# Kernel tuning notes

Hardware: AMD Instinct MI355X
Metric: run time of the kernel (lower is better)

## Reference

```python
import jax, jax.numpy as jnp
import numpy as np

X_LIST = [256, 256, 1024, 1024, 512]
LABEL_DIM = 8
MAX_SEQ_LEN = 64
B = 256
EMB = 128
ATTR = 64
HID = 512
LAYERS = 4


def setup_inputs() -> dict:
    key = jax.random.key(0)
    ki = iter(jax.random.split(key, 80))
    def nrm(shape):
        return jax.random.normal(next(ki), shape, jnp.float32) * 0.02
    inp = {}
    inp['label'] = jax.random.normal(next(ki), (B, LABEL_DIM), jnp.float32)
    inp['length'] = jax.random.randint(next(ki), (B,), 1, MAX_SEQ_LEN + 1)
    inp['x'] = jnp.stack([jax.random.randint(next(ki), (B, MAX_SEQ_LEN), 0, v) for v in X_LIST], axis=-1)
    inp['x_now'] = jnp.stack([jax.random.randint(next(ki), (B, MAX_SEQ_LEN), 0, v) for v in X_LIST], axis=-1)
    for i, v in enumerate(X_LIST):
        inp[f'emb{i}'] = nrm((v, EMB))
    inp['pad_emb'] = jnp.zeros((1, ATTR), jnp.float32)
    for i in range(len(X_LIST) - 1):
        inp[f'cond_W{i}'] = nrm((ATTR, (i + 1) * EMB))
        inp[f'cond_b{i}'] = jnp.zeros((ATTR,), jnp.float32)
    inp['len_W'] = nrm((64, MAX_SEQ_LEN))
    inp['len_b'] = jnp.zeros((64,), jnp.float32)
    comb_in = EMB * len(X_LIST) + 64  # 704
    inp['comb_W'] = nrm((LABEL_DIM, HID, comb_in))
    inp['comb_b'] = jnp.zeros((LABEL_DIM, HID), jnp.float32)
    inp['lstm_Wih'] = nrm((LAYERS, 4 * HID, HID))
    inp['lstm_Whh'] = nrm((LAYERS, 4 * HID, HID))
    inp['lstm_bih'] = jnp.zeros((LAYERS, 4 * HID), jnp.float32)
    inp['lstm_bhh'] = jnp.zeros((LAYERS, 4 * HID), jnp.float32)
    for i, v in enumerate(X_LIST):
        inp[f'out_W{i}'] = nrm((v, HID + ATTR))
        inp[f'out_b{i}'] = jnp.zeros((v,), jnp.float32)
    return inp


def _forward(label, emb0, emb1, emb2, emb3, emb4, pad_emb,
             cond_W0, cond_W1, cond_W2, cond_W3, cond_b0, cond_b1, cond_b2, cond_b3,
             len_W, len_b, comb_W, comb_b,
             lstm_Wih, lstm_Whh, lstm_bih, lstm_bhh,
             out_W0, out_W1, out_W2, out_W3, out_W4,
             out_b0, out_b1, out_b2, out_b3, out_b4,
             length, x, x_now):
    embs = [emb0, emb1, emb2, emb3, emb4]
    cond_W = [cond_W0, cond_W1, cond_W2, cond_W3]
    cond_b = [cond_b0, cond_b1, cond_b2, cond_b3]
    out_W = [out_W0, out_W1, out_W2, out_W3, out_W4]
    out_b = [out_b0, out_b1, out_b2, out_b3, out_b4]
    Bn, T, _ = x.shape
    # length branch: one_hot(length-1) -> Linear -> ReLU -> [B, 64]
    length_oh = jax.nn.one_hot(length - 1, MAX_SEQ_LEN, dtype=jnp.float32)
    length_out = jax.nn.relu(length_oh @ len_W.T + len_b)
    # per-attribute embedding lookups, concat -> [B, T, 5*128]
    emb_list = jnp.concatenate([embs[i][x[:, :, i]] for i in range(len(X_LIST))], axis=2)
    now_emb = jnp.concatenate([embs[i][x_now[:, :, i]] for i in range(len(X_LIST) - 1)], axis=2)
    # condition features: pad for head 0, small MLPs on prefixes of now_emb
    attr = [jnp.broadcast_to(pad_emb, (Bn, T, ATTR))]
    for i in range(len(X_LIST) - 1):
        attr.append(jax.nn.relu(now_emb[:, :, :(i + 1) * EMB] @ cond_W[i].T + cond_b[i]))
    combined = jnp.concatenate(
        [emb_list, jnp.broadcast_to(length_out[:, None, :], (Bn, T, 64))], axis=2)  # [B,T,704]
    # label-routed combine_fc: compute all LABEL_DIM branches, gather matching branch
    fc = jax.nn.relu(jnp.einsum('btd,lhd->blth', combined, comb_W) + comb_b[None, :, None, :])
    label_int = jnp.argmax(label, axis=1)
    combined_out = jnp.take_along_axis(fc, label_int[:, None, None, None], axis=1)[:, 0]  # [B,T,H]
    # 4-layer LSTM, torch gate order (i,f,g,o), zero initial state
    xs = combined_out.transpose(1, 0, 2)  # [T,B,H]
    for l in range(LAYERS):
        Wih_T = lstm_Wih[l].T
        Whh_T = lstm_Whh[l].T
        bias = lstm_bih[l] + lstm_bhh[l]
        def step(carry, xt, Wih_T=Wih_T, Whh_T=Whh_T, bias=bias):
            h, c = carry
            g = xt @ Wih_T + h @ Whh_T + bias
            gi, gf, gg, go = jnp.split(g, 4, axis=-1)
            c = jax.nn.sigmoid(gf) * c + jax.nn.sigmoid(gi) * jnp.tanh(gg)
            h = jax.nn.sigmoid(go) * jnp.tanh(c)
            return (h, c), h
        z = jnp.zeros((Bn, HID), xs.dtype)
        _, xs = jax.lax.scan(step, (z, z), xs)
    hidden = xs.transpose(1, 0, 2)  # [B,T,H]
    # per-attribute log-softmax heads over [hidden ; attr_i]
    preds = [jax.nn.log_softmax(
        jnp.concatenate([hidden, attr[i]], axis=-1) @ out_W[i].T + out_b[i], axis=-1)
        for i in range(len(X_LIST))]
    return jnp.concatenate(preds, axis=-1)  # [B, T, sum(X_LIST)]


def reference(label, emb0, emb1, emb2, emb3, emb4, pad_emb,
              cond_W0, cond_W1, cond_W2, cond_W3, cond_b0, cond_b1, cond_b2, cond_b3,
              len_W, len_b, comb_W, comb_b,
              lstm_Wih, lstm_Whh, lstm_bih, lstm_bhh,
              out_W0, out_W1, out_W2, out_W3, out_W4,
              out_b0, out_b1, out_b2, out_b3, out_b4,
              length, x, x_now):
    return _forward(label, emb0, emb1, emb2, emb3, emb4, pad_emb,
                    cond_W0, cond_W1, cond_W2, cond_W3, cond_b0, cond_b1, cond_b2, cond_b3,
                    len_W, len_b, comb_W, comb_b,
                    lstm_Wih, lstm_Whh, lstm_bih, lstm_bhh,
                    out_W0, out_W1, out_W2, out_W3, out_W4,
                    out_b0, out_b1, out_b2, out_b3, out_b4,
                    length, x, x_now)
```

## Files before the change

kernel.cpp:

```cpp
#include <hip/hip_runtime.h>
#include <math.h>


#define B_    256
#define T_    64
#define EMB_  128
#define HID_  512
#define G4_   2048
#define CIN_  704
#define HA_   576
#define ROW_  3072
#define OFF_HA 2048
#define OFF_HB 2560

#define WSUB_  256
#define WKC_   2048
#define HB0_   16384
#define SMEM_F 20480

#define BAR_T(tau) (64 + (tau) * 32)

struct Params {
  const float* label; const int* length; const int* x; const int* xnow;
  const float* emb[5]; const float* pad;
  const float* condW[4]; const float* condB[4];
  const float* lenW; const float* lenB;
  const float* combW; const float* combB;
  const float* Wih; const float* Whh; const float* bih; const float* bhh;
  const float* outW[5]; const float* outB[5];
  unsigned int* bar;
  float* out;
};

__device__ __forceinline__ void multi_barrier(unsigned int* cnt, unsigned int* gen,
                                              unsigned int n) {
  __syncthreads();
  if (threadIdx.x == 0) {
    unsigned int g = __hip_atomic_load(gen, __ATOMIC_RELAXED, __HIP_MEMORY_SCOPE_AGENT);
    unsigned int a = __hip_atomic_fetch_add(cnt, 1u, __ATOMIC_ACQ_REL, __HIP_MEMORY_SCOPE_AGENT);
    if (a == n - 1u) {
      __hip_atomic_store(cnt, 0u, __ATOMIC_RELAXED, __HIP_MEMORY_SCOPE_AGENT);
      __hip_atomic_store(gen, g + 1u, __ATOMIC_RELEASE, __HIP_MEMORY_SCOPE_AGENT);
    } else {
      while (__hip_atomic_load(gen, __ATOMIC_RELAXED, __HIP_MEMORY_SCOPE_AGENT) == g) {
        __builtin_amdgcn_s_sleep(2);
      }
      (void)__hip_atomic_load(gen, __ATOMIC_ACQUIRE, __HIP_MEMORY_SCOPE_AGENT);
    }
  }
  __syncthreads();
}

#define WRSLAB(SL) do { \
  _Pragma("unroll") \
  for (int qq = 0; qq < 8; ++qq) { \
    int cc = ((qq + lo) & 7) * 4; \
    *(float4*)&(SL)[lo * 32 + cc] = \
      make_float4(acc[qq][0], acc[qq][1], acc[qq][2], acc[qq][3]); \
  } } while (0)

#define RDSLAB(SL) do { \
  _Pragma("unroll") \
  for (int qq = 0; qq < 8; ++qq) { \
    int cc = ((qq + lo) & 7) * 4; \
    float4 vv = *(const float4*)&(SL)[lo * 32 + cc]; \
    acc[qq][0] += vv.x; acc[qq][1] += vv.y; \
    acc[qq][2] += vv.z; acc[qq][3] += vv.w; \
  } } while (0)

__global__ __launch_bounds__(256) void k_t1(Params P, int l) {
  __shared__ float sm[4608];
  const int out_off = (l & 1) ? OFF_HA : OFF_HB;
  const float* Wih = P.Wih + (size_t)l * G4_ * HID_;
  const int tid = threadIdx.x, blk = blockIdx.x;
  const int rt = blk >> 4, kt = blk & 15;
  const int r0 = rt * 128, k0 = kt * 32;
  const int ul = tid >> 3, kl = (tid & 7) * 4;
  #pragma unroll
  for (int p = 0; p < 4; ++p) {
    float4 v = *(const float4*)(Wih + (size_t)(r0 + p * 32 + ul) * HID_ + k0 + kl);
    *(float4*)&sm[(p * 32 + ul) * 36 + kl] = v;
  }
  __syncthreads();
  const int kk = tid >> 3, qb = (tid & 7) * 4;
  #pragma unroll
  for (int p = 0; p < 4; ++p) {
    int rl = qb + p * 32;
    float4 v = make_float4(sm[(rl + 0) * 36 + kk], sm[(rl + 1) * 36 + kk],
                           sm[(rl + 2) * 36 + kk], sm[(rl + 3) * 36 + kk]);
    int kabs = k0 + kk;
    int row = (r0 >> 8) * 256 + (kabs >> 1);
    int col = out_off + (kabs & 1) * 256 + (r0 & 255) + rl;
    *(float4*)&P.out[(size_t)row * ROW_ + col] = v;
  }
}

__global__ __launch_bounds__(256, 3) void k_gih(Params P, int l) {
  const int in_off  = (l & 1) ? OFF_HB : OFF_HA;
  const int out_off = (l & 1) ? OFF_HA : OFF_HB;
  const int tid = threadIdx.x;
  const int rg = tid & 63, mh = tid >> 6;
  const int rb = blockIdx.x >> 1, ch = blockIdx.x & 1;
  const int m_base = rb * 32;
  const float* arow[8];
  #pragma unroll
  for (int mm = 0; mm < 8; ++mm)
    arow[mm] = P.out + (size_t)(m_base + mh * 8 + mm) * ROW_ + in_off;
  for (int p0 = 0; p0 < 4; ++p0) {
    const int p = ch * 4 + p0;
    float acc[4][8];
    #pragma unroll
    for (int c = 0; c < 4; ++c)
      #pragma unroll
      for (int m = 0; m < 8; ++m) acc[c][m] = 0.f;
    const float* wp = P.out + (size_t)(p * 256) * ROW_ + out_off + rg * 4;
    for (int kq = 0; kq < 64; ++kq) {
      float4 w0 = *(const float4*)(wp);
      float4 w1 = *(const float4*)(wp + 256);
      float4 w2 = *(const float4*)(wp + ROW_);
      float4 w3 = *(const float4*)(wp + ROW_ + 256);
      #pragma unroll
      for (int mm = 0; mm < 8; ++mm) {
        float4 a = *(const float4*)(arow[mm] + kq * 4);
        acc[0][mm] += w0.x * a.x + w1.x * a.y + w2.x * a.z + w3.x * a.w;
        acc[1][mm] += w0.y * a.x + w1.y * a.y + w2.y * a.z + w3.y * a.w;
        acc[2][mm] += w0.z * a.x + w1.z * a.y + w2.z * a.z + w3.z * a.w;
        acc[3][mm] += w0.w * a.x + w1.w * a.y + w2.w * a.z + w3.w * a.w;
      }
      wp += 2 * ROW_;
    }
    int r4 = p * 256 + rg * 4;
    float4 bi = *(const float4*)(P.bih + l * G4_ + r4);
    float4 bh = *(const float4*)(P.bhh + l * G4_ + r4);
    float bx = bi.x + bh.x, by = bi.y + bh.y, bz = bi.z + bh.z, bw = bi.w + bh.w;
    #pragma unroll
    for (int mm = 0; mm < 8; ++mm) {
      int m = m_base + mh * 8 + mm;
      *(float4*)&P.out[(size_t)m * ROW_ + r4] =
        make_float4(acc[0][mm] + bx, acc[1][mm] + by,
                    acc[2][mm] + bz, acc[3][mm] + bw);
    }
  }
}

__global__ __launch_bounds__(256, 2) void k_lstmB(Params P, int l) {
  __shared__ float smem[SMEM_F];
  unsigned int* bar = P.bar;
  const int tid = threadIdx.x;
  const int blk = blockIdx.x;
  const int team = blk & 7, member = blk >> 3;
  const int out_off = (l & 1) ? OFF_HA : OFF_HB;

  const int kb  = tid >> 5;
  const int sgq = (tid >> 3) & 3;
  const int rg  = tid & 7;
  const bool owner = (tid < 32);
  const int s_base = team * 32 + sgq * 8;
  const int ucol0  = member * 8 + rg;

  {
    const float* Wl = P.Whh + (size_t)l * G4_ * HID_;
    const int r = tid >> 3, q = tid & 7;
    const float* src = Wl + (size_t)((r & 3) * 512 + member * 8 + (r >> 2)) * HID_
                       + q * 64;
    for (int j = 0; j < 16; ++j) {
      float4 v = *(const float4*)(src + j * 4);
      int k0 = q * 64 + j * 4;
      #pragma unroll
      for (int e = 0; e < 4; ++e) {
        int k = k0 + e;
        smem[(k >> 6) * WKC_ + ((k >> 3) & 7) * WSUB_ + (k & 7) * 32 + r] = (&v.x)[e];
      }
    }
  }
  __syncthreads();

  float cst[8];

  if (owner) {
    #pragma unroll
    for (int sj = 0; sj < 8; ++sj) {
      const size_t grow = (size_t)((s_base + sj) * 64 + 0) * ROW_;
      float zi = P.out[grow + 0 * 512 + ucol0];
      float zg = P.out[grow + 2 * 512 + ucol0];
      float zo = P.out[grow + 3 * 512 + ucol0];
      float si = 1.f / (1.f + expf(-zi));
      float so = 1.f / (1.f + expf(-zo));
      float cn = si * tanhf(zg);
      cst[sj] = cn;
      P.out[grow + out_off + ucol0] = so * tanhf(cn);
    }
  }

  for (int t = 1; t < T_; ++t) {
    multi_barrier(&bar[BAR_T(team)], &bar[BAR_T(team) + 16], 64);

    float Gp[8][4];
    if (owner) {
      #pragma unroll
      for (int sj = 0; sj < 8; ++sj) {
        const size_t grow = (size_t)((s_base + sj) * 64 + t) * ROW_;
        #pragma unroll
        for (int g = 0; g < 4; ++g)
          Gp[sj][g] = P.out[grow + g * 512 + ucol0];
      }
    }

    float acc[8][4];
    #pragma unroll
    for (int a = 0; a < 8; ++a)
      #pragma unroll
      for (int b = 0; b < 4; ++b) acc[a][b] = 0.f;

    const int idx0 = tid * 2, idx1 = idx0 + 1;
    const int s0 = idx0 >> 4, kq0 = idx0 & 15;
    const int s1 = idx1 >> 4, kq1 = idx1 & 15;
    const size_t hrow0 = (size_t)((team * 32 + s0) * 64 + (t - 1)) * ROW_ + out_off;
    const size_t hrow1 = (size_t)((team * 32 + s1) * 64 + (t - 1)) * ROW_ + out_off;
    const int c0 = s0 * 64 + ((kq0 * 4 + 8 * (s0 >> 3)) & 63);
    const int c1 = s1 * 64 + ((kq1 * 4 + 8 * (s1 >> 3)) & 63);
    {
      float4 v0 = *(const float4*)&P.out[hrow0 + kq0 * 4];
      float4 v1 = *(const float4*)&P.out[hrow1 + kq1 * 4];
      *(float4*)&smem[HB0_ + c0] = v0;
      *(float4*)&smem[HB0_ + c1] = v1;
    }
    __syncthreads();

    for (int kc = 0; kc < 8; ++kc) {
      float4 nv0 = make_float4(0.f, 0.f, 0.f, 0.f), nv1 = nv0;
      if (kc < 7) {
        nv0 = *(const float4*)&P.out[hrow0 + (kc + 1) * 64 + kq0 * 4];
        nv1 = *(const float4*)&P.out[hrow1 + (kc + 1) * 64 + kq1 * 4];
      }
      const float* wp  = &smem[kc * WKC_ + kb * WSUB_ + rg * 4];
      const float* hbv = &smem[HB0_ + (kc & 1) * 2048];
      #pragma unroll
      for (int kq2 = 0; kq2 < 2; ++kq2) {
        float4 h4[8];
        const int colr = kb * 8 + kq2 * 4;
        #pragma unroll
        for (int sj = 0; sj < 8; ++sj)
          h4[sj] = *(const float4*)&hbv[(sgq * 8 + sj) * 64 + ((colr + 8 * sgq) & 63)];
        #pragma unroll
        for (int e = 0; e < 4; ++e) {
          const float4 wv = *(const float4*)&wp[(kq2 * 4 + e) * 32];
          #pragma unroll
          for (int sj = 0; sj < 8; ++sj) {
            const float hv = (&h4[sj].x)[e];
            acc[sj][0] += hv * wv.x; acc[sj][1] += hv * wv.y;
            acc[sj][2] += hv * wv.z; acc[sj][3] += hv * wv.w;
          }
        }
      }
      if (kc < 7) {
        *(float4*)&smem[HB0_ + ((kc + 1) & 1) * 2048 + c0] = nv0;
        *(float4*)&smem[HB0_ + ((kc + 1) & 1) * 2048 + c1] = nv1;
      }
      __syncthreads();
    }

    #pragma unroll
    for (int a = 0; a < 8; ++a)
      #pragma unroll
      for (int b = 0; b < 4; ++b)
        acc[a][b] += __shfl_xor(acc[a][b], 32, 64);
    const int wv = tid >> 6;
    const bool halfLo = ((tid >> 5) & 1) == 0;
    const int lo = tid & 31;
    float* slab0 = &smem[HB0_];
    float* slab1 = &smem[HB0_ + 1024];
    if (halfLo && wv == 1) WRSLAB(slab0);
    if (halfLo && wv == 3) WRSLAB(slab1);
    __syncthreads();
    if (halfLo && wv == 0) RDSLAB(slab0);
    if (halfLo && wv == 2) RDSLAB(slab1);
    __syncthreads();
    if (halfLo && wv == 2) WRSLAB(slab0);
    __syncthreads();
    if (owner) {
      RDSLAB(slab0);
      #pragma unroll
      for (int sj = 0; sj < 8; ++sj) {
        const size_t orow = (size_t)((s_base + sj) * 64 + t) * ROW_;
        float zi = Gp[sj][0] + acc[sj][0];
        float zf = Gp[sj][1] + acc[sj][1];
        float zg = Gp[sj][2] + acc[sj][2];
        float zo = Gp[sj][3] + acc[sj][3];
        float si = 1.f / (1.f + expf(-zi));
        float sf = 1.f / (1.f + expf(-zf));
        float so = 1.f / (1.f + expf(-zo));
        float cn = sf * cst[sj] + si * tanhf(zg);
        cst[sj] = cn;
        P.out[orow + out_off + ucol0] = so * tanhf(cn);
      }
    }
  }
}

__global__ __launch_bounds__(256) void k_combine(Params P) {
  __shared__ float sA[16][CIN_];
  __shared__ float sLen[64];
  int b = blockIdx.x >> 2, t0 = (blockIdx.x & 3) * 16;
  int tid = threadIdx.x;
  int li = P.length[b] - 1;
  if (tid < 64) {
    float v = P.lenW[tid * 64 + li] + P.lenB[tid];
    sLen[tid] = v > 0.f ? v : 0.f;
  }
  float best = P.label[b * 8]; int l = 0;
  #pragma unroll
  for (int k = 1; k < 8; ++k) {
    float lv = P.label[b * 8 + k];
    if (lv > best) { best = lv; l = k; }
  }
  __syncthreads();
  for (int tt = 0; tt < 16; ++tt) {
    int t = t0 + tt;
    for (int k = tid; k < CIN_; k += 256) {
      float v;
      if (k < 640) {
        int a = k >> 7, e = k & 127;
        int xi = P.x[((b * T_ + t) * 5) + a];
        v = P.emb[a][xi * EMB_ + e];
      } else {
        v = sLen[k - 640];
      }
      sA[tt][k] = v;
    }
  }
  __syncthreads();
  int hg = tid & 127, mh = tid >> 7;
  int h = hg * 4, tb = mh * 8;
  const float* W0 = P.combW + ((size_t)(l * HID_ + h)) * CIN_;
  float acc[4][8];
  #pragma unroll
  for (int c = 0; c < 4; ++c)
    #pragma unroll
    for (int m = 0; m < 8; ++m) acc[c][m] = 0.f;
  for (int k = 0; k < CIN_; k += 4) {
    float4 w0 = *(const float4*)(const void*)(W0 + k);
    float4 w1 = *(const float4*)(const void*)(W0 + CIN_ + k);
    float4 w2 = *(const float4*)(const void*)(W0 + 2 * CIN_ + k);
    float4 w3 = *(const float4*)(const void*)(W0 + 3 * CIN_ + k);
    #pragma unroll
    for (int m = 0; m < 8; ++m) {
      float4 av = *(const float4*)&sA[tb + m][k];
      acc[0][m] += w0.x*av.x + w0.y*av.y + w0.z*av.z + w0.w*av.w;
      acc[1][m] += w1.x*av.x + w1.y*av.y + w1.z*av.z + w1.w*av.w;
      acc[2][m] += w2.x*av.x + w2.y*av.y + w2.z*av.z + w2.w*av.w;
      acc[3][m] += w3.x*av.x + w3.y*av.y + w3.z*av.z + w3.w*av.w;
    }
  }
  #pragma unroll
  for (int c = 0; c < 4; ++c) {
    float bias = P.combB[l * HID_ + h + c];
    #pragma unroll
    for (int m = 0; m < 8; ++m) {
      float v = acc[c][m] + bias;
      P.out[((size_t)(b * T_ + t0 + tb + m)) * ROW_ + OFF_HA + h + c] = v > 0.f ? v : 0.f;
    }
  }
}

template<int HEAD, int VH, int OFF>
__global__ __launch_bounds__(256, 2) void k_head(Params P) {
  __shared__ float sB[32][512];
  __shared__ float sAt[32][64];
  const int tid = threadIdx.x;
  const int m0 = blockIdx.x * 32;
  if (HEAD == 0) {
    for (int i = tid; i < 32 * 64; i += 256) sAt[i >> 6][i & 63] = P.pad[i & 63];
  } else {
    const int KA = HEAD * EMB_;
    for (int i = tid; i < 32 * KA; i += 256) {
      int tt = i / KA, k = i - tt * KA;
      int a = k >> 7, e = k & 127;
      int xi = P.xnow[((m0 + tt) * 5) + a];
      sB[tt][k] = P.emb[a][xi * EMB_ + e];
    }
    __syncthreads();
    int rg = tid >> 6, j = tid & 63;
    const float* Wr = P.condW[HEAD - 1] + (size_t)j * KA;
    float acc[8] = {0.f,0.f,0.f,0.f,0.f,0.f,0.f,0.f};
    for (int k = 0; k < KA; k += 4) {
      float4 w = *(const float4*)(const void*)(Wr + k);
      #pragma unroll
      for (int m = 0; m < 8; ++m) {
        float4 av = *(const float4*)&sB[rg * 8 + m][k];
        acc[m] += w.x*av.x + w.y*av.y + w.z*av.z + w.w*av.w;
      }
    }
    float bias = P.condB[HEAD - 1][j];
    #pragma unroll
    for (int m = 0; m < 8; ++m) {
      float v = acc[m] + bias;
      sAt[rg * 8 + m][j] = v > 0.f ? v : 0.f;
    }
    __syncthreads();
  }
  for (int i = tid; i < 32 * 512; i += 256) {
    int tt = i >> 9, k = i & 511;
    sB[tt][k] = P.out[((size_t)(m0 + tt)) * ROW_ + OFF_HA + k];
  }
  __syncthreads();
  constexpr int CG  = (VH >= 512) ? 128 : 64;
  constexpr int RPG = (VH >= 512) ? 16 : 8;
  const int cg = tid & (CG - 1), mh = tid / CG;
  const int tb = mh * RPG;
  const float* Wb = P.outW[HEAD];
  const float* bs = P.outB[HEAD];
  for (int c0 = cg * 4; c0 < VH; c0 += CG * 4) {
    const float* Wr = Wb + (size_t)c0 * HA_;
    float acc2[4][RPG];
    #pragma unroll
    for (int c = 0; c < 4; ++c)
      #pragma unroll
      for (int m = 0; m < RPG; ++m) acc2[c][m] = 0.f;
    for (int k = 0; k < 512; k += 4) {
      float4 w0 = *(const float4*)(const void*)(Wr + k);
      float4 w1 = *(const float4*)(const void*)(Wr + HA_ + k);
      float4 w2 = *(const float4*)(const void*)(Wr + 2 * HA_ + k);
      float4 w3 = *(const float4*)(const void*)(Wr + 3 * HA_ + k);
      #pragma unroll
      for (int m = 0; m < RPG; ++m) {
        float4 av = *(const float4*)&sB[tb + m][k];
        acc2[0][m] += w0.x*av.x + w0.y*av.y + w0.z*av.z + w0.w*av.w;
        acc2[1][m] += w1.x*av.x + w1.y*av.y + w1.z*av.z + w1.w*av.w;
        acc2[2][m] += w2.x*av.x + w2.y*av.y + w2.z*av.z + w2.w*av.w;
        acc2[3][m] += w3.x*av.x + w3.y*av.y + w3.z*av.z + w3.w*av.w;
      }
    }
    for (int k = 0; k < 64; k += 4) {
      float4 w0 = *(const float4*)(const void*)(Wr + 512 + k);
      float4 w1 = *(const float4*)(const void*)(Wr + HA_ + 512 + k);
      float4 w2 = *(const float4*)(const void*)(Wr + 2 * HA_ + 512 + k);
      float4 w3 = *(const float4*)(const void*)(Wr + 3 * HA_ + 512 + k);
      #pragma unroll
      for (int m = 0; m < RPG; ++m) {
        float4 av = *(const float4*)&sAt[tb + m][k];
        acc2[0][m] += w0.x*av.x + w0.y*av.y + w0.z*av.z + w0.w*av.w;
        acc2[1][m] += w1.x*av.x + w1.y*av.y + w1.z*av.z + w1.w*av.w;
        acc2[2][m] += w2.x*av.x + w2.y*av.y + w2.z*av.z + w2.w*av.w;
        acc2[3][m] += w3.x*av.x + w3.y*av.y + w3.z*av.z + w3.w*av.w;
      }
    }
    #pragma unroll
    for (int c = 0; c < 4; ++c) {
      float bi = bs[c0 + c];
      #pragma unroll
      for (int m = 0; m < RPG; ++m)
        P.out[((size_t)(m0 + tb + m)) * ROW_ + OFF + c0 + c] = acc2[c][m] + bi;
    }
  }
}

__global__ __launch_bounds__(256) void k_lsm(Params P) {
  __shared__ float sred[4];
  int m = blockIdx.x;
  float* row0 = P.out + (size_t)m * ROW_;
  int tid = threadIdx.x, lane = tid & 63, wid = tid >> 6;
  const int V[5] = {256, 256, 1024, 1024, 512};
  int off = 0;
  for (int head = 0; head < 5; ++head) {
    float* row = row0 + off; int Vh = V[head];
    float mx = -1e30f;
    for (int c = tid; c < Vh; c += 256) mx = fmaxf(mx, row[c]);
    for (int o = 32; o > 0; o >>= 1) mx = fmaxf(mx, __shfl_down(mx, o, 64));
    if (lane == 0) sred[wid] = mx;
    __syncthreads();
    mx = fmaxf(fmaxf(sred[0], sred[1]), fmaxf(sred[2], sred[3]));
    __syncthreads();
    float s = 0.f;
    for (int c = tid; c < Vh; c += 256) s += expf(row[c] - mx);
    for (int o = 32; o > 0; o >>= 1) s += __shfl_down(s, o, 64);
    if (lane == 0) sred[wid] = s;
    __syncthreads();
    float lse = mx + logf(sred[0] + sred[1] + sred[2] + sred[3]);
    __syncthreads();
    for (int c = tid; c < Vh; c += 256) row[c] = row[c] - lse;
    off += Vh;
  }
}

extern "C" void kernel_launch(void* const* d_in, const int* in_sizes, int n_in,
                              void* d_out, int out_size, void* d_ws, size_t ws_size,
                              hipStream_t stream) {
  (void)in_sizes; (void)n_in; (void)out_size; (void)ws_size;
  Params P;
  P.label  = (const float*)d_in[0];
  P.length = (const int*)  d_in[1];
  P.x      = (const int*)  d_in[2];
  P.xnow   = (const int*)  d_in[3];
  for (int i = 0; i < 5; ++i) P.emb[i] = (const float*)d_in[4 + i];
  P.pad = (const float*)d_in[9];
  for (int i = 0; i < 4; ++i) {
    P.condW[i] = (const float*)d_in[10 + 2 * i];
    P.condB[i] = (const float*)d_in[11 + 2 * i];
  }
  P.lenW  = (const float*)d_in[18]; P.lenB  = (const float*)d_in[19];
  P.combW = (const float*)d_in[20]; P.combB = (const float*)d_in[21];
  P.Wih   = (const float*)d_in[22]; P.Whh   = (const float*)d_in[23];
  P.bih   = (const float*)d_in[24]; P.bhh   = (const float*)d_in[25];
  for (int i = 0; i < 5; ++i) {
    P.outW[i] = (const float*)d_in[26 + 2 * i];
    P.outB[i] = (const float*)d_in[27 + 2 * i];
  }
  P.bar = (unsigned int*)d_ws;
  P.out = (float*)d_out;

  hipMemsetAsync(d_ws, 0, 1536, stream);
  k_combine<<<1024, 256, 0, stream>>>(P);
  for (int l = 0; l < 4; ++l) {
    k_t1 <<<256,  256, 0, stream>>>(P, l);
    k_gih<<<1024, 256, 0, stream>>>(P, l);
    void* args[] = { &P, &l };
    hipLaunchCooperativeKernel((void*)k_lstmB, dim3(512), dim3(256), args, 0, stream);
  }
  k_head<0,  256,    0><<<512, 256, 0, stream>>>(P);
  k_head<1,  256,  256><<<512, 256, 0, stream>>>(P);
  k_head<2, 1024,  512><<<512, 256, 0, stream>>>(P);
  k_head<4,  512, 2560><<<512, 256, 0, stream>>>(P);
  k_head<3, 1024, 1536><<<512, 256, 0, stream>>>(P);
  k_lsm<<<16384, 256, 0, stream>>>(P);
}
```

Measured before the change: 12.69 ms.

## Split LSTM teams into two ping-pong halves with monotonic arrival counters

Halves the recurrent LSTM grid to 256 blocks, each holding 16 hidden units' Whh slice, with more LDS and one block per CU. The 32 sequences of each team are split into two phases processed alternately. The generation-based team barrier is replaced by a monotonic per-phase arrival counter that each block polls, so one phase's recurrence can run while the other phase's peers are still finishing. This aims to cut barrier latency and hide synchronisation, at the cost of doubling per-block GEMV work and lowering occupancy.

```diff
diff --git a/kernel.cpp b/kernel.cpp
--- a/kernel.cpp
+++ b/kernel.cpp
@@ -13,12 +13,10 @@
 #define OFF_HA 2048
 #define OFF_HB 2560
 
-#define WSUB_  256
-#define WKC_   2048
-#define HB0_   16384
-#define SMEM_F 20480
-
-#define BAR_T(tau) (64 + (tau) * 32)
+#define WSUB_  516
+#define WKC_   4128
+#define HB0_   33024
+#define SMEM_F 35072
 
 struct Params {
   const float* label; const int* length; const int* x; const int* xnow;
@@ -32,25 +30,6 @@
   float* out;
 };
 
-__device__ __forceinline__ void multi_barrier(unsigned int* cnt, unsigned int* gen,
-                                              unsigned int n) {
-  __syncthreads();
-  if (threadIdx.x == 0) {
-    unsigned int g = __hip_atomic_load(gen, __ATOMIC_RELAXED, __HIP_MEMORY_SCOPE_AGENT);
-    unsigned int a = __hip_atomic_fetch_add(cnt, 1u, __ATOMIC_ACQ_REL, __HIP_MEMORY_SCOPE_AGENT);
-    if (a == n - 1u) {
-      __hip_atomic_store(cnt, 0u, __ATOMIC_RELAXED, __HIP_MEMORY_SCOPE_AGENT);
-      __hip_atomic_store(gen, g + 1u, __ATOMIC_RELEASE, __HIP_MEMORY_SCOPE_AGENT);
-    } else {
-      while (__hip_atomic_load(gen, __ATOMIC_RELAXED, __HIP_MEMORY_SCOPE_AGENT) == g) {
-        __builtin_amdgcn_s_sleep(2);
-      }
-      (void)__hip_atomic_load(gen, __ATOMIC_ACQUIRE, __HIP_MEMORY_SCOPE_AGENT);
-    }
-  }
-  __syncthreads();
-}
-
 #define WRSLAB(SL) do { \
   _Pragma("unroll") \
   for (int qq = 0; qq < 8; ++qq) { \
@@ -143,41 +122,13 @@
   }
 }
 
-__global__ __launch_bounds__(256, 2) void k_lstmB(Params P, int l) {
-  __shared__ float smem[SMEM_F];
-  unsigned int* bar = P.bar;
+__device__ __forceinline__ void lstm_t0(const Params& P, unsigned int* arrive,
+    int team, int member, int out_off, int sg, int rg, bool owner,
+    int ph, float (&cst)[8]) {
   const int tid = threadIdx.x;
-  const int blk = blockIdx.x;
-  const int team = blk & 7, member = blk >> 3;
-  const int out_off = (l & 1) ? OFF_HA : OFF_HB;
-
-  const int kb  = tid >> 5;
-  const int sgq = (tid >> 3) & 3;
-  const int rg  = tid & 7;
-  const bool owner = (tid < 32);
-  const int s_base = team * 32 + sgq * 8;
-  const int ucol0  = member * 8 + rg;
-
-  {
-    const float* Wl = P.Whh + (size_t)l * G4_ * HID_;
-    const int r = tid >> 3, q = tid & 7;
-    const float* src = Wl + (size_t)((r & 3) * 512 + member * 8 + (r >> 2)) * HID_
-                       + q * 64;
-    for (int j = 0; j < 16; ++j) {
-      float4 v = *(const float4*)(src + j * 4);
-      int k0 = q * 64 + j * 4;
-      #pragma unroll
-      for (int e = 0; e < 4; ++e) {
-        int k = k0 + e;
-        smem[(k >> 6) * WKC_ + ((k >> 3) & 7) * WSUB_ + (k & 7) * 32 + r] = (&v.x)[e];
-      }
-    }
-  }
-  __syncthreads();
-
-  float cst[8];
-
+  const int ucol0 = member * 16 + rg;
   if (owner) {
+    const int s_base = team * 32 + ph * 16 + sg * 8;
     #pragma unroll
     for (int sj = 0; sj < 8; ++sj) {
       const size_t grow = (size_t)((s_base + sj) * 64 + 0) * ROW_;
@@ -191,110 +142,157 @@
       P.out[grow + out_off + ucol0] = so * tanhf(cn);
     }
   }
-
+  __syncthreads();
+  if (tid == 0)
+    __hip_atomic_fetch_add(arrive, 1u, __ATOMIC_RELEASE, __HIP_MEMORY_SCOPE_AGENT);
+}
+
+__device__ __forceinline__ void lstm_step(const Params& P, float* smem,
+    unsigned int* arrive, unsigned int need, int t, int team, int member,
+    int out_off, int kb, int sg, int rg, bool owner, int ph, float (&cst)[8]) {
+  const int tid = threadIdx.x;
+  const int ucol0 = member * 16 + rg;
+  const int s_base = team * 32 + ph * 16 + sg * 8;
+
+  float Gp[8][4];
+  if (owner) {
+    #pragma unroll
+    for (int sj = 0; sj < 8; ++sj) {
+      const size_t grow = (size_t)((s_base + sj) * 64 + t) * ROW_;
+      #pragma unroll
+      for (int g = 0; g < 4; ++g)
+        Gp[sj][g] = P.out[grow + g * 512 + ucol0];
+    }
+  }
+
+  if (tid == 0) {
+    while (__hip_atomic_load(arrive, __ATOMIC_RELAXED, __HIP_MEMORY_SCOPE_AGENT) < need) {
+      __builtin_amdgcn_s_sleep(1);
+    }
+    (void)__hip_atomic_load(arrive, __ATOMIC_ACQUIRE, __HIP_MEMORY_SCOPE_AGENT);
+  }
+  __syncthreads();
+
+  float acc[8][4];
+  #pragma unroll
+  for (int a = 0; a < 8; ++a)
+    #pragma unroll
+    for (int b = 0; b < 4; ++b) acc[a][b] = 0.f;
+
+  const int sloc = tid >> 4, kq = tid & 15;
+  const size_t hrow = (size_t)((team * 32 + ph * 16 + sloc) * 64 + (t - 1)) * ROW_
+                      + out_off;
+  const int c = sloc * 64 + ((kq * 4 + 8 * (sloc >> 3)) & 63);
+  {
+    float4 v0 = *(const float4*)&P.out[hrow + kq * 4];
+    *(float4*)&smem[HB0_ + c] = v0;
+  }
+  __syncthreads();
+
+  for (int kc = 0; kc < 8; ++kc) {
+    float4 nv = make_float4(0.f, 0.f, 0.f, 0.f);
+    if (kc < 7)
+      nv = *(const float4*)&P.out[hrow + (kc + 1) * 64 + kq * 4];
+    const float* wp  = &smem[kc * WKC_ + kb * WSUB_ + rg * 4];
+    const float* hbv = &smem[HB0_ + (kc & 1) * 1024];
+    #pragma unroll
+    for (int kq2 = 0; kq2 < 2; ++kq2) {
+      float4 h4[8];
+      const int colr = kb * 8 + kq2 * 4;
+      #pragma unroll
+      for (int sj = 0; sj < 8; ++sj)
+        h4[sj] = *(const float4*)&hbv[(sg * 8 + sj) * 64 + ((colr + 8 * sg) & 63)];
+      #pragma unroll
+      for (int e = 0; e < 4; ++e) {
+        const float4 wv4 = *(const float4*)&wp[(kq2 * 4 + e) * 64];
+        #pragma unroll
+        for (int sj = 0; sj < 8; ++sj) {
+          const float hv = (&h4[sj].x)[e];
+          acc[sj][0] += hv * wv4.x; acc[sj][1] += hv * wv4.y;
+          acc[sj][2] += hv * wv4.z; acc[sj][3] += hv * wv4.w;
+        }
+      }
+    }
+    if (kc < 7)
+      *(float4*)&smem[HB0_ + ((kc + 1) & 1) * 1024 + c] = nv;
+    __syncthreads();
+  }
+
+  #pragma unroll
+  for (int a = 0; a < 8; ++a)
+    #pragma unroll
+    for (int b = 0; b < 4; ++b)
+      acc[a][b] += __shfl_xor(acc[a][b], 32, 64);
+  const int wv = tid >> 6;
+  const bool halfLo = ((tid >> 5) & 1) == 0;
+  const int lo = tid & 31;
+  float* slab0 = &smem[HB0_];
+  float* slab1 = &smem[HB0_ + 1024];
+  if (halfLo && wv == 1) WRSLAB(slab0);
+  if (halfLo && wv == 3) WRSLAB(slab1);
+  __syncthreads();
+  if (halfLo && wv == 0) RDSLAB(slab0);
+  if (halfLo && wv == 2) RDSLAB(slab1);
+  __syncthreads();
+  if (halfLo && wv == 2) WRSLAB(slab0);
+  __syncthreads();
+  if (owner) {
+    RDSLAB(slab0);
+    #pragma unroll
+    for (int sj = 0; sj < 8; ++sj) {
+      const size_t orow = (size_t)((s_base + sj) * 64 + t) * ROW_;
+      float zi = Gp[sj][0] + acc[sj][0];
+      float zf = Gp[sj][1] + acc[sj][1];
+      float zg = Gp[sj][2] + acc[sj][2];
+      float zo = Gp[sj][3] + acc[sj][3];
+      float si = 1.f / (1.f + expf(-zi));
+      float sf = 1.f / (1.f + expf(-zf));
+      float so = 1.f / (1.f + expf(-zo));
+      float cn = sf * cst[sj] + si * tanhf(zg);
+      cst[sj] = cn;
+      P.out[orow + out_off + ucol0] = so * tanhf(cn);
+    }
+  }
+  __syncthreads();
+  if (tid == 0)
+    __hip_atomic_fetch_add(arrive, 1u, __ATOMIC_RELEASE, __HIP_MEMORY_SCOPE_AGENT);
+}
+
+__global__ __launch_bounds__(256, 1) void k_lstmB(Params P, int l) {
+  __shared__ float smem[SMEM_F];
+  const int tid = threadIdx.x, blk = blockIdx.x;
+  const int team = blk & 7, member = blk >> 3;
+  const int out_off = (l & 1) ? OFF_HA : OFF_HB;
+  const int kb = tid >> 5, sg = (tid >> 4) & 1, rg = tid & 15;
+  const bool owner = (tid < 32);
+  unsigned int* arrA = P.bar + (1 + team) * 16;
+  unsigned int* arrB = P.bar + (9 + team) * 16;
+
+  {
+    const float* Wl = P.Whh + (size_t)l * G4_ * HID_;
+    const int r = tid >> 2, q = tid & 3;
+    const float* src = Wl + (size_t)((r & 3) * 512 + member * 16 + (r >> 2)) * HID_
+                       + q * 128;
+    for (int j = 0; j < 32; ++j) {
+      float4 v = *(const float4*)(src + j * 4);
+      int k0 = q * 128 + j * 4;
+      #pragma unroll
+      for (int e = 0; e < 4; ++e) {
+        int k = k0 + e;
+        smem[(k >> 6) * WKC_ + ((k >> 3) & 7) * WSUB_ + (k & 7) * 64 + r] = (&v.x)[e];
+      }
+    }
+  }
+  __syncthreads();
+
+  float cstA[8], cstB[8];
+  lstm_t0(P, arrA, team, member, out_off, sg, rg, owner, 0, cstA);
+  lstm_t0(P, arrB, team, member, out_off, sg, rg, owner, 1, cstB);
+  const unsigned int base = (unsigned int)l * 2048u;
   for (int t = 1; t < T_; ++t) {
-    multi_barrier(&bar[BAR_T(team)], &bar[BAR_T(team) + 16], 64);
-
-    float Gp[8][4];
-    if (owner) {
-      #pragma unroll
-      for (int sj = 0; sj < 8; ++sj) {
-        const size_t grow = (size_t)((s_base + sj) * 64 + t) * ROW_;
-        #pragma unroll
-        for (int g = 0; g < 4; ++g)
-          Gp[sj][g] = P.out[grow + g * 512 + ucol0];
-      }
-    }
-
-    float acc[8][4];
-    #pragma unroll
-    for (int a = 0; a < 8; ++a)
-      #pragma unroll
-      for (int b = 0; b < 4; ++b) acc[a][b] = 0.f;
-
-    const int idx0 = tid * 2, idx1 = idx0 + 1;
-    const int s0 = idx0 >> 4, kq0 = idx0 & 15;
-    const int s1 = idx1 >> 4, kq1 = idx1 & 15;
-    const size_t hrow0 = (size_t)((team * 32 + s0) * 64 + (t - 1)) * ROW_ + out_off;
-    const size_t hrow1 = (size_t)((team * 32 + s1) * 64 + (t - 1)) * ROW_ + out_off;
-    const int c0 = s0 * 64 + ((kq0 * 4 + 8 * (s0 >> 3)) & 63);
-    const int c1 = s1 * 64 + ((kq1 * 4 + 8 * (s1 >> 3)) & 63);
-    {
-      float4 v0 = *(const float4*)&P.out[hrow0 + kq0 * 4];
-      float4 v1 = *(const float4*)&P.out[hrow1 + kq1 * 4];
-      *(float4*)&smem[HB0_ + c0] = v0;
-      *(float4*)&smem[HB0_ + c1] = v1;
-    }
-    __syncthreads();
-
-    for (int kc = 0; kc < 8; ++kc) {
-      float4 nv0 = make_float4(0.f, 0.f, 0.f, 0.f), nv1 = nv0;
-      if (kc < 7) {
-        nv0 = *(const float4*)&P.out[hrow0 + (kc + 1) * 64 + kq0 * 4];
-        nv1 = *(const float4*)&P.out[hrow1 + (kc + 1) * 64 + kq1 * 4];
-      }
-      const float* wp  = &smem[kc * WKC_ + kb * WSUB_ + rg * 4];
-      const float* hbv = &smem[HB0_ + (kc & 1) * 2048];
-      #pragma unroll
-      for (int kq2 = 0; kq2 < 2; ++kq2) {
-        float4 h4[8];
-        const int colr = kb * 8 + kq2 * 4;
-        #pragma unroll
-        for (int sj = 0; sj < 8; ++sj)
-          h4[sj] = *(const float4*)&hbv[(sgq * 8 + sj) * 64 + ((colr + 8 * sgq) & 63)];
-        #pragma unroll
-        for (int e = 0; e < 4; ++e) {
-          const float4 wv = *(const float4*)&wp[(kq2 * 4 + e) * 32];
-          #pragma unroll
-          for (int sj = 0; sj < 8; ++sj) {
-            const float hv = (&h4[sj].x)[e];
-            acc[sj][0] += hv * wv.x; acc[sj][1] += hv * wv.y;
-            acc[sj][2] += hv * wv.z; acc[sj][3] += hv * wv.w;
-          }
-        }
-      }
-      if (kc < 7) {
-        *(float4*)&smem[HB0_ + ((kc + 1) & 1) * 2048 + c0] = nv0;
-        *(float4*)&smem[HB0_ + ((kc + 1) & 1) * 2048 + c1] = nv1;
-      }
-      __syncthreads();
-    }
-
-    #pragma unroll
-    for (int a = 0; a < 8; ++a)
-      #pragma unroll
-      for (int b = 0; b < 4; ++b)
-        acc[a][b] += __shfl_xor(acc[a][b], 32, 64);
-    const int wv = tid >> 6;
-    const bool halfLo = ((tid >> 5) & 1) == 0;
-    const int lo = tid & 31;
-    float* slab0 = &smem[HB0_];
-    float* slab1 = &smem[HB0_ + 1024];
-    if (halfLo && wv == 1) WRSLAB(slab0);
-    if (halfLo && wv == 3) WRSLAB(slab1);
-    __syncthreads();
-    if (halfLo && wv == 0) RDSLAB(slab0);
-    if (halfLo && wv == 2) RDSLAB(slab1);
-    __syncthreads();
-    if (halfLo && wv == 2) WRSLAB(slab0);
-    __syncthreads();
-    if (owner) {
-      RDSLAB(slab0);
-      #pragma unroll
-      for (int sj = 0; sj < 8; ++sj) {
-        const size_t orow = (size_t)((s_base + sj) * 64 + t) * ROW_;
-        float zi = Gp[sj][0] + acc[sj][0];
-        float zf = Gp[sj][1] + acc[sj][1];
-        float zg = Gp[sj][2] + acc[sj][2];
-        float zo = Gp[sj][3] + acc[sj][3];
-        float si = 1.f / (1.f + expf(-zi));
-        float sf = 1.f / (1.f + expf(-zf));
-        float so = 1.f / (1.f + expf(-zo));
-        float cn = sf * cst[sj] + si * tanhf(zg);
-        cst[sj] = cn;
-        P.out[orow + out_off + ucol0] = so * tanhf(cn);
-      }
-    }
+    const unsigned int need = base + 32u * (unsigned int)t;
+    lstm_step(P, smem, arrA, need, t, team, member, out_off, kb, sg, rg, owner, 0, cstA);
+    lstm_step(P, smem, arrB, need, t, team, member, out_off, kb, sg, rg, owner, 1, cstB);
   }
 }
 
@@ -515,7 +513,7 @@
     k_t1 <<<256,  256, 0, stream>>>(P, l);
     k_gih<<<1024, 256, 0, stream>>>(P, l);
     void* args[] = { &P, &l };
-    hipLaunchCooperativeKernel((void*)k_lstmB, dim3(512), dim3(256), args, 0, stream);
+    hipLaunchCooperativeKernel((void*)k_lstmB, dim3(256), dim3(256), args, 0, stream);
   }
   k_head<0,  256,    0><<<512, 256, 0, stream>>>(P);
   k_head<1,  256,  256><<<512, 256, 0, stream>>>(P);
```

Result: no change. 12.45 ms (-1.9%).
